# Kernel optimization log

Hardware: AMD Instinct MI355X
Metric: run time of the kernel (lower is better)

The kernel has to match this reference:

```python
import jax, jax.numpy as jnp
import numpy as np

BS, N, C_IMG, C_PT, H, W = 8, 100000, 512, 256, 48, 160


def setup_inputs() -> dict:
    key = jax.random.key(0)
    ks = jax.random.split(key, 8)
    point_feat = jax.random.normal(ks[0], (N, C_PT), dtype=jnp.float32)
    # pillar centers in LiDAR frame: x forward [10,60], y left [-10,10], z [-2,1]
    u = jax.random.uniform(ks[1], (N, 3), dtype=jnp.float32)
    pillar_centers = jnp.stack([
        10.0 + 50.0 * u[:, 0],
        -10.0 + 20.0 * u[:, 1],
        -2.0 + 3.0 * u[:, 2],
    ], axis=1)
    batch_idx = jax.random.randint(ks[2], (N,), 0, BS, dtype=jnp.int32)
    img_feat = jax.random.normal(ks[3], (BS, C_IMG, H, W), dtype=jnp.float32)
    # KITTI-style calibration (per batch, small jitter)
    f, cx, cy = 80.0, 80.0, 24.0
    P2_base = np.array([[f, 0, cx, 0], [0, f, cy, 0], [0, 0, 1, 0]], dtype=np.float32)
    Tr_base = np.array([[0, -1, 0, 0], [0, 0, -1, 0], [1, 0, 0, 0], [0, 0, 0, 1]], dtype=np.float32)
    rng = np.random.RandomState(0)
    P2 = np.stack([P2_base + 0.01 * rng.randn(3, 4).astype(np.float32) for _ in range(BS)])
    R0 = np.stack([np.eye(4, dtype=np.float32) for _ in range(BS)])
    Tr = np.stack([Tr_base + 0.001 * rng.randn(4, 4).astype(np.float32) for _ in range(BS)])
    align_w = jax.random.normal(ks[4], (C_PT, C_IMG), dtype=jnp.float32) * 0.02
    align_b = jax.random.normal(ks[5], (C_PT,), dtype=jnp.float32) * 0.02
    return {
        'point_feat': point_feat, 'pillar_centers': pillar_centers,
        'img_feat': img_feat, 'P2': jnp.asarray(P2), 'R0': jnp.asarray(R0),
        'Tr': jnp.asarray(Tr), 'align_w': align_w, 'align_b': align_b,
        'batch_idx': batch_idx, 'img_h': H, 'img_w': W,
    }


def _fuse(point_feat, pillar_centers, img_feat, P2, R0, Tr, align_w, align_b,
          batch_idx, img_h, img_w):
    n = point_feat.shape[0]
    dt = point_feat.dtype
    # --- project_to_image (vectorized over all points via per-point calib gather) ---
    pts_hom = jnp.concatenate([pillar_centers, jnp.ones((n, 1), dtype=dt)], axis=1)  # [N,4]
    pts_cam = jnp.einsum('nij,nj->ni', Tr[batch_idx], pts_hom)    # [N,4]
    pts_rect = jnp.einsum('nij,nj->ni', R0[batch_idx], pts_cam)   # [N,4]
    pts_img = jnp.einsum('nij,nj->ni', P2[batch_idx], pts_rect)   # [N,3]
    depth = jnp.clip(pts_img[:, 2:3], 1e-5, None)
    uv = pts_img[:, :2] / depth
    valid = ((pts_img[:, 2] > 0) & (uv[:, 0] >= 0) & (uv[:, 0] < img_w)
             & (uv[:, 1] >= 0) & (uv[:, 1] < img_h))
    # --- grid_sample bilinear, align_corners=True, padding_mode='zeros' ---
    # grid = 2*uv/(dim-1)-1 with align_corners=True => pixel coords == uv.
    _, C, Hf, Wf = img_feat.shape
    u_, v_ = uv[:, 0], uv[:, 1]
    x0 = jnp.floor(u_); y0 = jnp.floor(v_)
    wx1 = u_ - x0; wx0 = 1.0 - wx1
    wy1 = v_ - y0; wy0 = 1.0 - wy1

    def gather(xi, yi):
        inb = (xi >= 0) & (xi <= Wf - 1) & (yi >= 0) & (yi <= Hf - 1)
        xc = jnp.clip(xi, 0, Wf - 1).astype(jnp.int32)
        yc = jnp.clip(yi, 0, Hf - 1).astype(jnp.int32)
        f = img_feat[batch_idx, :, yc, xc]  # [N,C]
        return f * inb.astype(dt)[:, None]

    sampled = (gather(x0, y0) * (wx0 * wy0)[:, None]
               + gather(x0 + 1, y0) * (wx1 * wy0)[:, None]
               + gather(x0, y0 + 1) * (wx0 * wy1)[:, None]
               + gather(x0 + 1, y0 + 1) * (wx1 * wy1)[:, None])
    sampled = jnp.where(valid[:, None], sampled, jnp.zeros((), dtype=dt))
    # --- align (Linear) + residual add ---
    aligned = sampled @ align_w.T + align_b
    return point_feat + aligned


def reference(point_feat, pillar_centers, img_feat, P2, R0, Tr, align_w, align_b,
              batch_idx, img_h, img_w):
    return _fuse(point_feat, pillar_centers, img_feat, P2, R0, Tr,
                 align_w, align_b, batch_idx, img_h, img_w)
```

## Files before the change

### kernel.cpp

```cpp
#include <hip/hip_runtime.h>

#define C_IMG 512
#define C_PT  256
#define IMG_H 48
#define IMG_W 160
#define HWPIX (IMG_H * IMG_W)

#define MP   64
#define BK   64
#define SPAD 72

typedef short bf16x8 __attribute__((ext_vector_type(8)));
typedef float f32x4  __attribute__((ext_vector_type(4)));

static __device__ __forceinline__ unsigned short f2bf(float f) {
    unsigned u = __float_as_uint(f);
    u += 0x7fffu + ((u >> 16) & 1u);
    return (unsigned short)(u >> 16);
}
static __device__ __forceinline__ unsigned pack2(float lo, float hi) {
    return (unsigned)f2bf(lo) | ((unsigned)f2bf(hi) << 16);
}
static __device__ __forceinline__ float bflo(unsigned v) { return __uint_as_float(v << 16); }
static __device__ __forceinline__ float bfhi(unsigned v) { return __uint_as_float(v & 0xffff0000u); }

__global__ __launch_bounds__(256)
void transpose_kernel(const float* __restrict__ img, unsigned short* __restrict__ imgT) {
    __shared__ float tile[32][33];
    const int b   = blockIdx.z;
    const int hw0 = blockIdx.x * 32;
    const int c0  = blockIdx.y * 32;
    const int tx  = threadIdx.x;
    const int ty  = threadIdx.y;
    const float* src = img + (size_t)b * C_IMG * HWPIX;
    #pragma unroll
    for (int i = 0; i < 32; i += 8)
        tile[ty + i][tx] = src[(size_t)(c0 + ty + i) * HWPIX + hw0 + tx];
    __syncthreads();
    unsigned short* dst = imgT + (size_t)b * HWPIX * C_IMG;
    #pragma unroll
    for (int i = 0; i < 32; i += 8)
        dst[(size_t)(hw0 + ty + i) * C_IMG + c0 + tx] = f2bf(tile[tx][ty + i]);
}

template<bool TRANS>
__global__ __launch_bounds__(256)
void fused_kernel(const float* __restrict__ pf,
                  const float* __restrict__ centers,
                  const void*  __restrict__ imgv,
                  const float* __restrict__ P2,
                  const float* __restrict__ R0,
                  const float* __restrict__ Tr,
                  const float* __restrict__ alw,
                  const float* __restrict__ alb,
                  const int*   __restrict__ bidx,
                  float* __restrict__ out,
                  int n)
{
    __shared__ float          sWg[MP][4];
    __shared__ int            sOf[MP][4];
    __shared__ unsigned short sS[MP][SPAD];
    __shared__ unsigned short sW[C_PT][SPAD];

    const int tid = threadIdx.x;
    const int pt0 = blockIdx.x * MP;

    if (tid < MP) {
        const int p = pt0 + tid;
        float w[4] = {0.f, 0.f, 0.f, 0.f};
        int   o[4] = {0, 0, 0, 0};
        if (p < n) {
            const float cx = centers[p * 3 + 0];
            const float cy = centers[p * 3 + 1];
            const float cz = centers[p * 3 + 2];
            const int   b  = bidx[p];
            const float* tr = Tr + b * 16;
            const float c0 = tr[0]*cx + tr[1]*cy + tr[2]*cz + tr[3];
            const float c1 = tr[4]*cx + tr[5]*cy + tr[6]*cz + tr[7];
            const float c2 = tr[8]*cx + tr[9]*cy + tr[10]*cz + tr[11];
            const float c3 = tr[12]*cx + tr[13]*cy + tr[14]*cz + tr[15];
            const float* r0 = R0 + b * 16;
            const float e0 = r0[0]*c0 + r0[1]*c1 + r0[2]*c2 + r0[3]*c3;
            const float e1 = r0[4]*c0 + r0[5]*c1 + r0[6]*c2 + r0[7]*c3;
            const float e2 = r0[8]*c0 + r0[9]*c1 + r0[10]*c2 + r0[11]*c3;
            const float e3 = r0[12]*c0 + r0[13]*c1 + r0[14]*c2 + r0[15]*c3;
            const float* p2 = P2 + b * 12;
            const float ix = p2[0]*e0 + p2[1]*e1 + p2[2]*e2  + p2[3]*e3;
            const float iy = p2[4]*e0 + p2[5]*e1 + p2[6]*e2  + p2[7]*e3;
            const float iz = p2[8]*e0 + p2[9]*e1 + p2[10]*e2 + p2[11]*e3;
            const float depth = fmaxf(iz, 1e-5f);
            const float u = ix / depth;
            const float v = iy / depth;
            const bool valid = (iz > 0.f) && (u >= 0.f) && (u < (float)IMG_W)
                                         && (v >= 0.f) && (v < (float)IMG_H);
            const float x0f = floorf(u), y0f = floorf(v);
            const float wx1 = u - x0f, wx0 = 1.f - wx1;
            const float wy1 = v - y0f, wy0 = 1.f - wy1;
            const float cw[4] = {wx0 * wy0, wx1 * wy0, wx0 * wy1, wx1 * wy1};
            #pragma unroll
            for (int j = 0; j < 4; ++j) {
                const float xf = x0f + (float)(j & 1);
                const float yf = y0f + (float)(j >> 1);
                const bool inb = (xf >= 0.f) && (xf <= (float)(IMG_W - 1))
                              && (yf >= 0.f) && (yf <= (float)(IMG_H - 1));
                const int xc = (int)fminf(fmaxf(xf, 0.f), (float)(IMG_W - 1));
                const int yc = (int)fminf(fmaxf(yf, 0.f), (float)(IMG_H - 1));
                w[j] = (valid && inb) ? cw[j] : 0.f;
                o[j] = TRANS ? ((b * IMG_H + yc) * IMG_W + xc) * C_IMG
                             : b * C_IMG * HWPIX + yc * IMG_W + xc;
            }
        }
        #pragma unroll
        for (int j = 0; j < 4; ++j) { sWg[tid][j] = w[j]; sOf[tid][j] = o[j]; }
    }

    f32x4 acc[4][4];
    #pragma unroll
    for (int i = 0; i < 4; ++i)
        #pragma unroll
        for (int j = 0; j < 4; ++j)
            acc[i][j] = (f32x4){0.f, 0.f, 0.f, 0.f};

    const int lane = tid & 63;
    const int wid  = tid >> 6;
    const int l15  = lane & 15;
    const int quad = lane >> 4;
    const int sp   = tid >> 2;
    const int ssub = tid & 3;

    __syncthreads();

    for (int ck = 0; ck < C_IMG / BK; ++ck) {
        {
            const float cw0 = sWg[sp][0], cw1 = sWg[sp][1], cw2 = sWg[sp][2], cw3 = sWg[sp][3];
            const int   co0 = sOf[sp][0], co1 = sOf[sp][1], co2 = sOf[sp][2], co3 = sOf[sp][3];
            const int   cb  = ck * BK + ssub * 16;
            if (TRANS) {
                const unsigned short* ib = (const unsigned short*)imgv;
                #pragma unroll
                for (int h = 0; h < 2; ++h) {
                    const uint4 q0 = *(const uint4*)(ib + co0 + cb + h * 8);
                    const uint4 q1 = *(const uint4*)(ib + co1 + cb + h * 8);
                    const uint4 q2 = *(const uint4*)(ib + co2 + cb + h * 8);
                    const uint4 q3 = *(const uint4*)(ib + co3 + cb + h * 8);
                    const unsigned* u0 = (const unsigned*)&q0;
                    const unsigned* u1 = (const unsigned*)&q1;
                    const unsigned* u2 = (const unsigned*)&q2;
                    const unsigned* u3 = (const unsigned*)&q3;
                    uint4 ov;
                    unsigned* op = (unsigned*)&ov;
                    #pragma unroll
                    for (int wI = 0; wI < 4; ++wI) {
                        const float vlo = cw0*bflo(u0[wI]) + cw1*bflo(u1[wI]) + cw2*bflo(u2[wI]) + cw3*bflo(u3[wI]);
                        const float vhi = cw0*bfhi(u0[wI]) + cw1*bfhi(u1[wI]) + cw2*bfhi(u2[wI]) + cw3*bfhi(u3[wI]);
                        op[wI] = pack2(vlo, vhi);
                    }
                    *(uint4*)&sS[sp][ssub * 16 + h * 8] = ov;
                }
            } else {
                const float* ib = (const float*)imgv;
                #pragma unroll
                for (int h = 0; h < 2; ++h) {
                    uint4 ov;
                    unsigned* op = (unsigned*)&ov;
                    #pragma unroll
                    for (int wI = 0; wI < 4; ++wI) {
                        const int c = cb + h * 8 + 2 * wI;
                        const float vlo = cw0*ib[co0 + c*HWPIX] + cw1*ib[co1 + c*HWPIX]
                                        + cw2*ib[co2 + c*HWPIX] + cw3*ib[co3 + c*HWPIX];
                        const float vhi = cw0*ib[co0 + (c+1)*HWPIX] + cw1*ib[co1 + (c+1)*HWPIX]
                                        + cw2*ib[co2 + (c+1)*HWPIX] + cw3*ib[co3 + (c+1)*HWPIX];
                        op[wI] = pack2(vlo, vhi);
                    }
                    *(uint4*)&sS[sp][ssub * 16 + h * 8] = ov;
                }
            }
        }
        {
            #pragma unroll
            for (int pass = 0; pass < 4; ++pass) {
                const int r = pass * 64 + (tid >> 2);
                const int c = (tid & 3) * 16;
                const float* wr = alw + (size_t)r * C_IMG + ck * BK + c;
                const float4 f0 = *(const float4*)(wr + 0);
                const float4 f1 = *(const float4*)(wr + 4);
                const float4 f2 = *(const float4*)(wr + 8);
                const float4 f3 = *(const float4*)(wr + 12);
                uint4 oa, ob;
                oa.x = pack2(f0.x, f0.y); oa.y = pack2(f0.z, f0.w);
                oa.z = pack2(f1.x, f1.y); oa.w = pack2(f1.z, f1.w);
                ob.x = pack2(f2.x, f2.y); ob.y = pack2(f2.z, f2.w);
                ob.z = pack2(f3.x, f3.y); ob.w = pack2(f3.z, f3.w);
                *(uint4*)&sW[r][c]     = oa;
                *(uint4*)&sW[r][c + 8] = ob;
            }
        }
        __syncthreads();

        #pragma unroll
        for (int kk = 0; kk < 2; ++kk) {
            bf16x8 af[4], bfr[4];
            #pragma unroll
            for (int mt = 0; mt < 4; ++mt)
                af[mt] = *(const bf16x8*)&sS[mt * 16 + l15][kk * 32 + quad * 8];
            #pragma unroll
            for (int nt = 0; nt < 4; ++nt)
                bfr[nt] = *(const bf16x8*)&sW[wid * 64 + nt * 16 + l15][kk * 32 + quad * 8];
            #pragma unroll
            for (int mt = 0; mt < 4; ++mt)
                #pragma unroll
                for (int nt = 0; nt < 4; ++nt)
                    acc[mt][nt] = __builtin_amdgcn_mfma_f32_16x16x32_bf16(
                        af[mt], bfr[nt], acc[mt][nt], 0, 0, 0);
        }
        __syncthreads();
    }

    #pragma unroll
    for (int mt = 0; mt < 4; ++mt) {
        #pragma unroll
        for (int r = 0; r < 4; ++r) {
            const int p = pt0 + mt * 16 + quad * 4 + r;
            if (p < n) {
                #pragma unroll
                for (int nt = 0; nt < 4; ++nt) {
                    const int nc = wid * 64 + nt * 16 + l15;
                    const size_t idx = (size_t)p * C_PT + nc;
                    out[idx] = pf[idx] + alb[nc] + acc[mt][nt][r];
                }
            }
        }
    }
}

extern "C" void kernel_launch(void* const* d_in, const int* in_sizes, int n_in,
                              void* d_out, int out_size, void* d_ws, size_t ws_size,
                              hipStream_t stream) {
    const float* pf      = (const float*)d_in[0];
    const float* centers = (const float*)d_in[1];
    const float* img     = (const float*)d_in[2];
    const float* P2      = (const float*)d_in[3];
    const float* R0      = (const float*)d_in[4];
    const float* Tr      = (const float*)d_in[5];
    const float* alw     = (const float*)d_in[6];
    const float* alb     = (const float*)d_in[7];
    const int*   bidx    = (const int*)d_in[8];
    float*       out     = (float*)d_out;

    const int n  = in_sizes[8];
    const int bs = in_sizes[3] / 12;
    const int nblk = (n + MP - 1) / MP;

    const size_t tneed = (size_t)bs * HWPIX * C_IMG * sizeof(unsigned short);
    if (ws_size >= tneed) {
        unsigned short* imgT = (unsigned short*)d_ws;
        dim3 tg(HWPIX / 32, C_IMG / 32, bs);
        transpose_kernel<<<tg, dim3(32, 8), 0, stream>>>(img, imgT);
        fused_kernel<true><<<nblk, 256, 0, stream>>>(
            pf, centers, (const void*)imgT, P2, R0, Tr, alw, alb, bidx, out, n);
    } else {
        fused_kernel<false><<<nblk, 256, 0, stream>>>(
            pf, centers, (const void*)img, P2, R0, Tr, alw, alb, bidx, out, n);
    }
}
```

Before: 408.3 us.

## Pre-convert weights to bf16, double-buffer gathers, read B fragments from global

A separate kernel now converts align_w to bf16 once per call, and the fused kernel reads MFMA B fragments straight from global/L2, so the per-block shared-memory weight tile and its conversion disappear. The image gather for the next K chunk is issued before the MFMAs on the current chunk, using a double-buffered shared sample tile to hide gather latency. The transpose kernel moves to 64-channel tiles with packed 32-bit bf16 stores, and the launch bound asks for 3 blocks per CU. The trade-off is more register pressure from the in-flight gather registers, plus uncoalesced global B loads that rely on L2 hits.

```diff
diff --git a/kernel.cpp b/kernel.cpp
--- a/kernel.cpp
+++ b/kernel.cpp
@@ -26,41 +26,84 @@
 
 __global__ __launch_bounds__(256)
 void transpose_kernel(const float* __restrict__ img, unsigned short* __restrict__ imgT) {
-    __shared__ float tile[32][33];
+    __shared__ float tile[64][33];
     const int b   = blockIdx.z;
     const int hw0 = blockIdx.x * 32;
-    const int c0  = blockIdx.y * 32;
+    const int c0  = blockIdx.y * 64;
     const int tx  = threadIdx.x;
     const int ty  = threadIdx.y;
     const float* src = img + (size_t)b * C_IMG * HWPIX;
     #pragma unroll
-    for (int i = 0; i < 32; i += 8)
+    for (int i = 0; i < 64; i += 8)
         tile[ty + i][tx] = src[(size_t)(c0 + ty + i) * HWPIX + hw0 + tx];
     __syncthreads();
-    unsigned short* dst = imgT + (size_t)b * HWPIX * C_IMG;
-    #pragma unroll
-    for (int i = 0; i < 32; i += 8)
-        dst[(size_t)(hw0 + ty + i) * C_IMG + c0 + tx] = f2bf(tile[tx][ty + i]);
-}
-
-template<bool TRANS>
+    unsigned* dst = (unsigned*)(imgT + (size_t)b * HWPIX * C_IMG);
+    #pragma unroll
+    for (int i = 0; i < 32; i += 8) {
+        const int hw = ty + i;
+        dst[(size_t)(hw0 + hw) * (C_IMG / 2) + (c0 >> 1) + tx] =
+            pack2(tile[2 * tx][hw], tile[2 * tx + 1][hw]);
+    }
+}
+
 __global__ __launch_bounds__(256)
-void fused_kernel(const float* __restrict__ pf,
-                  const float* __restrict__ centers,
-                  const void*  __restrict__ imgv,
-                  const float* __restrict__ P2,
-                  const float* __restrict__ R0,
-                  const float* __restrict__ Tr,
-                  const float* __restrict__ alw,
-                  const float* __restrict__ alb,
-                  const int*   __restrict__ bidx,
-                  float* __restrict__ out,
-                  int n)
+void cvt_w_kernel(const float* __restrict__ alw, unsigned short* __restrict__ alwT) {
+    const int i = (blockIdx.x * 256 + threadIdx.x) * 8;
+    const float4 a = *(const float4*)(alw + i);
+    const float4 b = *(const float4*)(alw + i + 4);
+    uint4 o;
+    o.x = pack2(a.x, a.y); o.y = pack2(a.z, a.w);
+    o.z = pack2(b.x, b.y); o.w = pack2(b.z, b.w);
+    *(uint4*)(alwT + i) = o;
+}
+
+static __device__ __forceinline__ void gather_issue(
+    const unsigned short* __restrict__ ib, const int* co, int cb, uint4* g)
+{
+    #pragma unroll
+    for (int c = 0; c < 4; ++c) {
+        g[2 * c]     = *(const uint4*)(ib + co[c] + cb);
+        g[2 * c + 1] = *(const uint4*)(ib + co[c] + cb + 8);
+    }
+}
+static __device__ __forceinline__ void gather_commit(
+    unsigned short* __restrict__ dst, const uint4* g, const float* cw)
+{
+    #pragma unroll
+    for (int h = 0; h < 2; ++h) {
+        const unsigned* u0 = (const unsigned*)&g[0 + h];
+        const unsigned* u1 = (const unsigned*)&g[2 + h];
+        const unsigned* u2 = (const unsigned*)&g[4 + h];
+        const unsigned* u3 = (const unsigned*)&g[6 + h];
+        uint4 ov; unsigned* op = (unsigned*)&ov;
+        #pragma unroll
+        for (int wI = 0; wI < 4; ++wI) {
+            const float vlo = cw[0]*bflo(u0[wI]) + cw[1]*bflo(u1[wI])
+                            + cw[2]*bflo(u2[wI]) + cw[3]*bflo(u3[wI]);
+            const float vhi = cw[0]*bfhi(u0[wI]) + cw[1]*bfhi(u1[wI])
+                            + cw[2]*bfhi(u2[wI]) + cw[3]*bfhi(u3[wI]);
+            op[wI] = pack2(vlo, vhi);
+        }
+        *(uint4*)(dst + h * 8) = ov;
+    }
+}
+
+__global__ __launch_bounds__(256, 3)
+void fused_trans_kernel(const float* __restrict__ pf,
+                        const float* __restrict__ centers,
+                        const unsigned short* __restrict__ imgT,
+                        const unsigned short* __restrict__ alwT,
+                        const float* __restrict__ P2,
+                        const float* __restrict__ R0,
+                        const float* __restrict__ Tr,
+                        const float* __restrict__ alb,
+                        const int*   __restrict__ bidx,
+                        float* __restrict__ out,
+                        int n)
 {
     __shared__ float          sWg[MP][4];
     __shared__ int            sOf[MP][4];
-    __shared__ unsigned short sS[MP][SPAD];
-    __shared__ unsigned short sW[C_PT][SPAD];
+    __shared__ unsigned short sS[2][MP][SPAD];
 
     const int tid = threadIdx.x;
     const int pt0 = blockIdx.x * MP;
@@ -96,7 +139,7 @@
             const float x0f = floorf(u), y0f = floorf(v);
             const float wx1 = u - x0f, wx0 = 1.f - wx1;
             const float wy1 = v - y0f, wy0 = 1.f - wy1;
-            const float cw[4] = {wx0 * wy0, wx1 * wy0, wx0 * wy1, wx1 * wy1};
+            const float cwv[4] = {wx0 * wy0, wx1 * wy0, wx0 * wy1, wx1 * wy1};
             #pragma unroll
             for (int j = 0; j < 4; ++j) {
                 const float xf = x0f + (float)(j & 1);
@@ -105,9 +148,8 @@
                               && (yf >= 0.f) && (yf <= (float)(IMG_H - 1));
                 const int xc = (int)fminf(fmaxf(xf, 0.f), (float)(IMG_W - 1));
                 const int yc = (int)fminf(fmaxf(yf, 0.f), (float)(IMG_H - 1));
-                w[j] = (valid && inb) ? cw[j] : 0.f;
-                o[j] = TRANS ? ((b * IMG_H + yc) * IMG_W + xc) * C_IMG
-                             : b * C_IMG * HWPIX + yc * IMG_W + xc;
+                w[j] = (valid && inb) ? cwv[j] : 0.f;
+                o[j] = ((b * IMG_H + yc) * IMG_W + xc) * C_IMG;
             }
         }
         #pragma unroll
@@ -130,50 +172,171 @@
 
     __syncthreads();
 
+    float cw[4]; int co[4];
+    #pragma unroll
+    for (int j = 0; j < 4; ++j) { cw[j] = sWg[sp][j]; co[j] = sOf[sp][j]; }
+    const int cbase = ssub * 16;
+
+    const unsigned short* bwp = alwT + (size_t)(wid * 64 + l15) * C_IMG + quad * 8;
+
+    {
+        uint4 g0[8];
+        gather_issue(imgT, co, cbase, g0);
+        gather_commit(&sS[0][sp][cbase], g0, cw);
+    }
+    __syncthreads();
+
+    #pragma unroll
+    for (int ck = 0; ck < C_IMG / BK; ++ck) {
+        const int cur = ck & 1;
+        uint4 gn[8];
+        if (ck < C_IMG / BK - 1)
+            gather_issue(imgT, co, (ck + 1) * BK + cbase, gn);
+
+        #pragma unroll
+        for (int kk = 0; kk < 2; ++kk) {
+            bf16x8 bfr[4], af[4];
+            #pragma unroll
+            for (int nt = 0; nt < 4; ++nt)
+                bfr[nt] = *(const bf16x8*)(bwp + nt * 16 * C_IMG + ck * BK + kk * 32);
+            #pragma unroll
+            for (int mt = 0; mt < 4; ++mt)
+                af[mt] = *(const bf16x8*)&sS[cur][mt * 16 + l15][kk * 32 + quad * 8];
+            #pragma unroll
+            for (int mt = 0; mt < 4; ++mt)
+                #pragma unroll
+                for (int nt = 0; nt < 4; ++nt)
+                    acc[mt][nt] = __builtin_amdgcn_mfma_f32_16x16x32_bf16(
+                        af[mt], bfr[nt], acc[mt][nt], 0, 0, 0);
+        }
+
+        if (ck < C_IMG / BK - 1)
+            gather_commit(&sS[cur ^ 1][sp][cbase], gn, cw);
+        __syncthreads();
+    }
+
+    #pragma unroll
+    for (int mt = 0; mt < 4; ++mt) {
+        #pragma unroll
+        for (int r = 0; r < 4; ++r) {
+            const int p = pt0 + mt * 16 + quad * 4 + r;
+            if (p < n) {
+                #pragma unroll
+                for (int nt = 0; nt < 4; ++nt) {
+                    const int nc = wid * 64 + nt * 16 + l15;
+                    const size_t idx = (size_t)p * C_PT + nc;
+                    out[idx] = pf[idx] + alb[nc] + acc[mt][nt][r];
+                }
+            }
+        }
+    }
+}
+
+__global__ __launch_bounds__(256)
+void fused_fallback_kernel(const float* __restrict__ pf,
+                           const float* __restrict__ centers,
+                           const float* __restrict__ img,
+                           const float* __restrict__ P2,
+                           const float* __restrict__ R0,
+                           const float* __restrict__ Tr,
+                           const float* __restrict__ alw,
+                           const float* __restrict__ alb,
+                           const int*   __restrict__ bidx,
+                           float* __restrict__ out,
+                           int n)
+{
+    __shared__ float          sWg[MP][4];
+    __shared__ int            sOf[MP][4];
+    __shared__ unsigned short sS[MP][SPAD];
+    __shared__ unsigned short sW[C_PT][SPAD];
+
+    const int tid = threadIdx.x;
+    const int pt0 = blockIdx.x * MP;
+
+    if (tid < MP) {
+        const int p = pt0 + tid;
+        float w[4] = {0.f, 0.f, 0.f, 0.f};
+        int   o[4] = {0, 0, 0, 0};
+        if (p < n) {
+            const float cx = centers[p * 3 + 0];
+            const float cy = centers[p * 3 + 1];
+            const float cz = centers[p * 3 + 2];
+            const int   b  = bidx[p];
+            const float* tr = Tr + b * 16;
+            const float c0 = tr[0]*cx + tr[1]*cy + tr[2]*cz + tr[3];
+            const float c1 = tr[4]*cx + tr[5]*cy + tr[6]*cz + tr[7];
+            const float c2 = tr[8]*cx + tr[9]*cy + tr[10]*cz + tr[11];
+            const float c3 = tr[12]*cx + tr[13]*cy + tr[14]*cz + tr[15];
+            const float* r0 = R0 + b * 16;
+            const float e0 = r0[0]*c0 + r0[1]*c1 + r0[2]*c2 + r0[3]*c3;
+            const float e1 = r0[4]*c0 + r0[5]*c1 + r0[6]*c2 + r0[7]*c3;
+            const float e2 = r0[8]*c0 + r0[9]*c1 + r0[10]*c2 + r0[11]*c3;
+            const float e3 = r0[12]*c0 + r0[13]*c1 + r0[14]*c2 + r0[15]*c3;
+            const float* p2 = P2 + b * 12;
+            const float ix = p2[0]*e0 + p2[1]*e1 + p2[2]*e2  + p2[3]*e3;
+            const float iy = p2[4]*e0 + p2[5]*e1 + p2[6]*e2  + p2[7]*e3;
+            const float iz = p2[8]*e0 + p2[9]*e1 + p2[10]*e2 + p2[11]*e3;
+            const float depth = fmaxf(iz, 1e-5f);
+            const float u = ix / depth;
+            const float v = iy / depth;
+            const bool valid = (iz > 0.f) && (u >= 0.f) && (u < (float)IMG_W)
+                                         && (v >= 0.f) && (v < (float)IMG_H);
+            const float x0f = floorf(u), y0f = floorf(v);
+            const float wx1 = u - x0f, wx0 = 1.f - wx1;
+            const float wy1 = v - y0f, wy0 = 1.f - wy1;
+            const float cwv[4] = {wx0 * wy0, wx1 * wy0, wx0 * wy1, wx1 * wy1};
+            #pragma unroll
+            for (int j = 0; j < 4; ++j) {
+                const float xf = x0f + (float)(j & 1);
+                const float yf = y0f + (float)(j >> 1);
+                const bool inb = (xf >= 0.f) && (xf <= (float)(IMG_W - 1))
+                              && (yf >= 0.f) && (yf <= (float)(IMG_H - 1));
+                const int xc = (int)fminf(fmaxf(xf, 0.f), (float)(IMG_W - 1));
+                const int yc = (int)fminf(fmaxf(yf, 0.f), (float)(IMG_H - 1));
+                w[j] = (valid && inb) ? cwv[j] : 0.f;
+                o[j] = b * C_IMG * HWPIX + yc * IMG_W + xc;
+            }
+        }
+        #pragma unroll
+        for (int j = 0; j < 4; ++j) { sWg[tid][j] = w[j]; sOf[tid][j] = o[j]; }
+    }
+
+    f32x4 acc[4][4];
+    #pragma unroll
+    for (int i = 0; i < 4; ++i)
+        #pragma unroll
+        for (int j = 0; j < 4; ++j)
+            acc[i][j] = (f32x4){0.f, 0.f, 0.f, 0.f};
+
+    const int lane = tid & 63;
+    const int wid  = tid >> 6;
+    const int l15  = lane & 15;
+    const int quad = lane >> 4;
+    const int sp   = tid >> 2;
+    const int ssub = tid & 3;
+
+    __syncthreads();
+
     for (int ck = 0; ck < C_IMG / BK; ++ck) {
         {
             const float cw0 = sWg[sp][0], cw1 = sWg[sp][1], cw2 = sWg[sp][2], cw3 = sWg[sp][3];
             const int   co0 = sOf[sp][0], co1 = sOf[sp][1], co2 = sOf[sp][2], co3 = sOf[sp][3];
             const int   cb  = ck * BK + ssub * 16;
-            if (TRANS) {
-                const unsigned short* ib = (const unsigned short*)imgv;
+            const float* ib = img;
+            #pragma unroll
+            for (int h = 0; h < 2; ++h) {
+                uint4 ov;
+                unsigned* op = (unsigned*)&ov;
                 #pragma unroll
-                for (int h = 0; h < 2; ++h) {
-                    const uint4 q0 = *(const uint4*)(ib + co0 + cb + h * 8);
-                    const uint4 q1 = *(const uint4*)(ib + co1 + cb + h * 8);
-                    const uint4 q2 = *(const uint4*)(ib + co2 + cb + h * 8);
-                    const uint4 q3 = *(const uint4*)(ib + co3 + cb + h * 8);
-                    const unsigned* u0 = (const unsigned*)&q0;
-                    const unsigned* u1 = (const unsigned*)&q1;
-                    const unsigned* u2 = (const unsigned*)&q2;
-                    const unsigned* u3 = (const unsigned*)&q3;
-                    uint4 ov;
-                    unsigned* op = (unsigned*)&ov;
-                    #pragma unroll
-                    for (int wI = 0; wI < 4; ++wI) {
-                        const float vlo = cw0*bflo(u0[wI]) + cw1*bflo(u1[wI]) + cw2*bflo(u2[wI]) + cw3*bflo(u3[wI]);
-                        const float vhi = cw0*bfhi(u0[wI]) + cw1*bfhi(u1[wI]) + cw2*bfhi(u2[wI]) + cw3*bfhi(u3[wI]);
-                        op[wI] = pack2(vlo, vhi);
-                    }
-                    *(uint4*)&sS[sp][ssub * 16 + h * 8] = ov;
+                for (int wI = 0; wI < 4; ++wI) {
+                    const int c = cb + h * 8 + 2 * wI;
+                    const float vlo = cw0*ib[co0 + c*HWPIX] + cw1*ib[co1 + c*HWPIX]
+                                    + cw2*ib[co2 + c*HWPIX] + cw3*ib[co3 + c*HWPIX];
+                    const float vhi = cw0*ib[co0 + (c+1)*HWPIX] + cw1*ib[co1 + (c+1)*HWPIX]
+                                    + cw2*ib[co2 + (c+1)*HWPIX] + cw3*ib[co3 + (c+1)*HWPIX];
+                    op[wI] = pack2(vlo, vhi);
                 }
-            } else {
-                const float* ib = (const float*)imgv;
-                #pragma unroll
-                for (int h = 0; h < 2; ++h) {
-                    uint4 ov;
-                    unsigned* op = (unsigned*)&ov;
-                    #pragma unroll
-                    for (int wI = 0; wI < 4; ++wI) {
-                        const int c = cb + h * 8 + 2 * wI;
-                        const float vlo = cw0*ib[co0 + c*HWPIX] + cw1*ib[co1 + c*HWPIX]
-                                        + cw2*ib[co2 + c*HWPIX] + cw3*ib[co3 + c*HWPIX];
-                        const float vhi = cw0*ib[co0 + (c+1)*HWPIX] + cw1*ib[co1 + (c+1)*HWPIX]
-                                        + cw2*ib[co2 + (c+1)*HWPIX] + cw3*ib[co3 + (c+1)*HWPIX];
-                        op[wI] = pack2(vlo, vhi);
-                    }
-                    *(uint4*)&sS[sp][ssub * 16 + h * 8] = ov;
-                }
+                *(uint4*)&sS[sp][ssub * 16 + h * 8] = ov;
             }
         }
         {
@@ -251,15 +414,17 @@
     const int bs = in_sizes[3] / 12;
     const int nblk = (n + MP - 1) / MP;
 
-    const size_t tneed = (size_t)bs * HWPIX * C_IMG * sizeof(unsigned short);
-    if (ws_size >= tneed) {
+    const size_t timg = (size_t)bs * HWPIX * C_IMG * sizeof(unsigned short);
+    const size_t tw   = (size_t)C_PT * C_IMG * sizeof(unsigned short);
+    if (ws_size >= timg + tw) {
         unsigned short* imgT = (unsigned short*)d_ws;
-        dim3 tg(HWPIX / 32, C_IMG / 32, bs);
-        transpose_kernel<<<tg, dim3(32, 8), 0, stream>>>(img, imgT);
-        fused_kernel<true><<<nblk, 256, 0, stream>>>(
-            pf, centers, (const void*)imgT, P2, R0, Tr, alw, alb, bidx, out, n);
+        unsigned short* alwT = (unsigned short*)((char*)d_ws + timg);
+        transpose_kernel<<<dim3(HWPIX / 32, C_IMG / 64, bs), dim3(32, 8), 0, stream>>>(img, imgT);
+        cvt_w_kernel<<<dim3((C_PT * C_IMG / 8) / 256), 256, 0, stream>>>(alw, alwT);
+        fused_trans_kernel<<<nblk, 256, 0, stream>>>(
+            pf, centers, imgT, alwT, P2, R0, Tr, alb, bidx, out, n);
     } else {
-        fused_kernel<false><<<nblk, 256, 0, stream>>>(
-            pf, centers, (const void*)img, P2, R0, Tr, alw, alb, bidx, out, n);
-    }
-}
+        fused_fallback_kernel<<<nblk, 256, 0, stream>>>(
+            pf, centers, img, P2, R0, Tr, alw, alb, bidx, out, n);
+    }
+}
```

Result: faster. 396.3 us (-2.9%).
